# Performance work log

Hardware: AMD Instinct MI355X
Metric: run time of the kernel (lower is better)

## Reference

```python
import jax, jax.numpy as jnp
import numpy as np

B, S, DIN, DQ, DK = 8, 2048, 1024, 64, 64

def setup_inputs() -> dict:
    key = jax.random.key(0)
    ks = jax.random.split(key, 8)
    sc = 0.02
    return {
        "input_tensor": jax.random.normal(ks[0], (B, S, DIN), jnp.float32),
        "attention_mask": jax.random.randint(ks[1], (B, 1, S), 0, 2) == 1,
        "Wq": jax.random.normal(ks[2], (DIN, DQ), jnp.float32) * sc,
        "bq": jnp.zeros((DQ,), jnp.float32),
        "Wk": jax.random.normal(ks[3], (DIN, DK), jnp.float32) * sc,
        "bk": jnp.zeros((DK,), jnp.float32),
        "Wv": jax.random.normal(ks[4], (DIN, DK), jnp.float32) * sc,
        "bv": jnp.zeros((DK,), jnp.float32),
    }

def reference(input_tensor, attention_mask, Wq, bq, Wk, bk, Wv, bv):
    q = input_tensor @ Wq + bq          # [B,S,DQ]
    k = input_tensor @ Wk + bk          # [B,S,DK]
    v = input_tensor @ Wv + bv          # [B,S,DK]
    # NOTE: original scales by sqrt(query.size(1)) == sqrt(seq_len), faithfully kept
    scale = q.shape[1] ** 0.5
    scores = jnp.einsum('bqd,bkd->bqk', q, k) / scale
    scores = jnp.where(attention_mask, jnp.float32(-1e9), scores)
    attn = jax.nn.softmax(scores, axis=-1)
    context = jnp.einsum('bqk,bkd->bqd', attn, v)
    return context
```

## Files before the change

kernel.cpp:

```cpp
#include <hip/hip_runtime.h>
#include <hip/hip_bf16.h>

#define NB 8
#define SEQ 2048
#define DIN 1024
#define DH 64

typedef __attribute__((ext_vector_type(8))) short bf16x8;
typedef __attribute__((ext_vector_type(4))) float f32x4;
typedef __attribute__((ext_vector_type(4))) unsigned int u32x4;

static __device__ __forceinline__ unsigned short f2bf(float f) {
    unsigned int u = __builtin_bit_cast(unsigned int, f);
    unsigned int r = (u + 0x7FFFu + ((u >> 16) & 1u)) >> 16;
    return (unsigned short)r;
}

static __device__ __forceinline__ unsigned int cvt_pk_bf16(float lo, float hi) {
    unsigned int d;
    asm volatile("v_cvt_pk_bf16_f32 %0, %1, %2" : "=v"(d) : "v"(lo), "v"(hi));
    return d;
}

static __device__ __forceinline__ void gll16(const void* g, void* l) {
    __builtin_amdgcn_global_load_lds((const __attribute__((address_space(1))) unsigned int*)g,
                                     (__attribute__((address_space(3))) unsigned int*)l, 16, 0, 0);
}

#define WAITVM(N) asm volatile("s_waitcnt vmcnt(" #N ")" ::: "memory")

__global__ __launch_bounds__(256) void prep_kernel(
    const float* __restrict__ Wq, const float* __restrict__ Wk, const float* __restrict__ Wv,
    unsigned short* __restrict__ Wfrag)
{
    int j = blockIdx.x * 256 + threadIdx.x;
    int mat = j >> 16;
    int rem = j & 65535;
    int k = rem >> 6;
    int c = rem & 63;
    const float* W = (mat == 0) ? Wq : ((mat == 1) ? Wk : Wv);
    float v = W[rem];
    int col = mat * 64 + c;
    int cg = col >> 4, cl = col & 15;
    int kk = k >> 5, kq = (k >> 3) & 3, ke = k & 7;
    Wfrag[(size_t)(kk * 12 + cg) * 512 + cl * 32 + kq * 8 + ke] = f2bf(v);
}

__global__ __launch_bounds__(256) void qkv_kernel(
    const float* __restrict__ X, const unsigned short* __restrict__ Wfrag,
    const float* __restrict__ bq, const float* __restrict__ bk, const float* __restrict__ bv,
    unsigned short* __restrict__ Qb, unsigned short* __restrict__ Kb, unsigned short* __restrict__ Vt)
{
    __shared__ __align__(16) unsigned char Xs[3][8192];
    __shared__ __align__(16) unsigned char Ws[2][24576];

    const int tid = threadIdx.x;
    const int w   = tid >> 6;
    const int l15 = tid & 15;
    const int lq  = (tid >> 4) & 3;
    const int row0 = blockIdx.x * 32;

    const char* Xg = (const char*)(X + (size_t)row0 * DIN);
    const char* Wg = (const char*)Wfrag;

    int xlds[2], xsrc[2];
    #pragma unroll
    for (int i = 0; i < 2; ++i) {
        int b = i * 4096 + tid * 16;
        int row = b >> 8;
        int g = (b >> 4) & 15;
        xlds[i] = b;
        xsrc[i] = row * 4096 + (g ^ (row & 7)) * 16;
    }

    f32x4 acc[2][3] = {};

    #pragma unroll
    for (int i = 0; i < 2; ++i) gll16(Xg + (size_t)xsrc[i], &Xs[0][xlds[i]]);
    #pragma unroll
    for (int i = 0; i < 6; ++i) gll16(Wg + (size_t)(i * 4096 + tid * 16), &Ws[0][i * 4096 + tid * 16]);
    #pragma unroll
    for (int i = 0; i < 2; ++i) gll16(Xg + (size_t)xsrc[i] + 256, &Xs[1][xlds[i]]);

    #pragma unroll
    for (int t = 0; t < 16; ++t) {
        if (t < 15) { WAITVM(2); } else { WAITVM(0); }
        __builtin_amdgcn_s_barrier();
        __builtin_amdgcn_sched_barrier(0);

        if (t + 1 < 16) {
            #pragma unroll
            for (int i = 0; i < 6; ++i)
                gll16(Wg + (size_t)(t + 1) * 24576 + i * 4096 + tid * 16,
                      &Ws[(t + 1) & 1][i * 4096 + tid * 16]);
        }
        if (t + 2 < 16) {
            #pragma unroll
            for (int i = 0; i < 2; ++i)
                gll16(Xg + (size_t)xsrc[i] + (t + 2) * 256, &Xs[(t + 2) % 3][xlds[i]]);
        }

        const unsigned char* xb = Xs[t % 3];
        const unsigned char* wt = Ws[t & 1];
        #pragma unroll
        for (int kk = 0; kk < 2; ++kk) {
            bf16x8 a[2];
            #pragma unroll
            for (int m = 0; m < 2; ++m) {
                int row = m * 16 + l15;
                const unsigned char* rp = xb + row * 256;
                f32x4 f0 = *(const f32x4*)(rp + ((kk * 8 + lq * 2 + 0) ^ (row & 7)) * 16);
                f32x4 f1 = *(const f32x4*)(rp + ((kk * 8 + lq * 2 + 1) ^ (row & 7)) * 16);
                u32x4 pk;
                pk[0] = cvt_pk_bf16(f0[0], f0[1]);
                pk[1] = cvt_pk_bf16(f0[2], f0[3]);
                pk[2] = cvt_pk_bf16(f1[0], f1[1]);
                pk[3] = cvt_pk_bf16(f1[2], f1[3]);
                a[m] = __builtin_bit_cast(bf16x8, pk);
            }
            #pragma unroll
            for (int n = 0; n < 3; ++n) {
                bf16x8 bf = *(const bf16x8*)(wt + (kk * 12 + w * 3 + n) * 1024 + (l15 * 4 + lq) * 16);
                acc[0][n] = __builtin_amdgcn_mfma_f32_16x16x32_bf16(a[0], bf, acc[0][n], 0, 0, 0);
                acc[1][n] = __builtin_amdgcn_mfma_f32_16x16x32_bf16(a[1], bf, acc[1][n], 0, 0, 0);
            }
        }
    }

    #pragma unroll
    for (int n = 0; n < 3; ++n) {
        int col = w * 48 + n * 16 + l15;
        int mat = col >> 6, c = col & 63;
        float badd = ((mat == 0) ? bq : ((mat == 1) ? bk : bv))[c];
        #pragma unroll
        for (int m = 0; m < 2; ++m) {
            #pragma unroll
            for (int reg = 0; reg < 4; ++reg) {
                int row = row0 + m * 16 + lq * 4 + reg;
                unsigned short v16 = f2bf(acc[m][n][reg] + badd);
                if (mat == 0)      Qb[(size_t)row * DH + c] = v16;
                else if (mat == 1) Kb[(size_t)row * DH + c] = v16;
                else {
                    int bb = row >> 11, ss = row & 2047;
                    Vt[((size_t)(bb * DH + c)) * SEQ + ss] = v16;
                }
            }
        }
    }
}

#define AKT 64
#define ANT 8
#define PP 36

__global__ __launch_bounds__(256) void attn_kernel(
    const unsigned short* __restrict__ Qb, const unsigned short* __restrict__ Kb,
    const unsigned short* __restrict__ Vt, const int* __restrict__ mask,
    float* __restrict__ Opart, float* __restrict__ lpart)
{
    __shared__ __align__(16) unsigned char Ksm[3][8192];
    __shared__ __align__(16) unsigned char Vsm[3][8192];
    __shared__ short ps[4][32][PP];
    __shared__ float sml[4][32];

    const int tid = threadIdx.x;
    const int w   = tid >> 6;
    const int l15 = tid & 15;
    const int lq  = (tid >> 4) & 3;
    const int wm  = w >> 1;
    const int wn  = w & 1;

    int bid = blockIdx.x;
    int sbid = (bid & 7) * 128 + (bid >> 3);
    const int b   = sbid >> 7;
    const int qt  = (sbid >> 2) & 31;
    const int kq  = sbid & 3;
    const int q0  = qt * 64;
    const int kb0 = kq * 512;

    bf16x8 aq[2][2];
    #pragma unroll
    for (int m = 0; m < 2; ++m)
        #pragma unroll
        for (int kk = 0; kk < 2; ++kk)
            aq[m][kk] = *(const bf16x8*)(Qb + ((size_t)(b * SEQ + q0 + wm * 32 + m * 16 + l15)) * DH + kk * 32 + lq * 8);

    int mk[ANT][2];
    #pragma unroll
    for (int t = 0; t < ANT; ++t) {
        mk[t][0] = mask[b * SEQ + kb0 + t * AKT + wn * 32 + l15];
        mk[t][1] = mask[b * SEQ + kb0 + t * AKT + wn * 32 + 16 + l15];
    }
    WAITVM(0);

    const char* Kg = (const char*)Kb + (size_t)(b * SEQ + kb0) * DH * 2;
    const char* Vg = (const char*)Vt + ((size_t)(b * DH) * SEQ + kb0) * 2;

    int slds[2], ksrc[2], vsrc[2];
    #pragma unroll
    for (int i = 0; i < 2; ++i) {
        int bb = i * 4096 + tid * 16;
        int row = bb >> 7;
        int g = (bb >> 4) & 7;
        int gs = g ^ (row & 7);
        slds[i] = bb;
        ksrc[i] = row * 128 + gs * 16;
        vsrc[i] = row * 4096 + gs * 16;
    }

    f32x4 o[2][4];
    #pragma unroll
    for (int m = 0; m < 2; ++m)
        #pragma unroll
        for (int n = 0; n < 4; ++n) o[m][n] = f32x4{0, 0, 0, 0};
    float lr[2][4] = {};
    const float rscale = 0.022097086912079612f;

    #pragma unroll
    for (int i = 0; i < 2; ++i) gll16(Kg + (size_t)ksrc[i], &Ksm[0][slds[i]]);
    #pragma unroll
    for (int i = 0; i < 2; ++i) gll16(Vg + (size_t)vsrc[i], &Vsm[0][slds[i]]);
    #pragma unroll
    for (int i = 0; i < 2; ++i) gll16(Kg + (size_t)8192 + ksrc[i], &Ksm[1][slds[i]]);
    #pragma unroll
    for (int i = 0; i < 2; ++i) gll16(Vg + (size_t)128 + vsrc[i], &Vsm[1][slds[i]]);

    #pragma unroll
    for (int t = 0; t < ANT; ++t) {
        if (t < ANT - 1) { WAITVM(4); } else { WAITVM(0); }
        __builtin_amdgcn_s_barrier();
        __builtin_amdgcn_sched_barrier(0);

        if (t + 2 < ANT) {
            int bi = (t + 2) % 3;
            #pragma unroll
            for (int i = 0; i < 2; ++i) gll16(Kg + (size_t)(t + 2) * 8192 + ksrc[i], &Ksm[bi][slds[i]]);
            #pragma unroll
            for (int i = 0; i < 2; ++i) gll16(Vg + (size_t)(t + 2) * 128 + vsrc[i], &Vsm[bi][slds[i]]);
        }

        const unsigned char* kt  = Ksm[t % 3];
        const unsigned char* vt2 = Vsm[t % 3];

        bf16x8 bkf[2][2];
        #pragma unroll
        for (int n = 0; n < 2; ++n)
            #pragma unroll
            for (int kk = 0; kk < 2; ++kk) {
                int row = wn * 32 + n * 16 + l15;
                bkf[n][kk] = *(const bf16x8*)(kt + row * 128 + ((4 * kk + lq) ^ (row & 7)) * 16);
            }
        f32x4 s[2][2];
        #pragma unroll
        for (int m = 0; m < 2; ++m)
            #pragma unroll
            for (int n = 0; n < 2; ++n) s[m][n] = f32x4{0, 0, 0, 0};
        #pragma unroll
        for (int kk = 0; kk < 2; ++kk)
            #pragma unroll
            for (int m = 0; m < 2; ++m)
                #pragma unroll
                for (int n = 0; n < 2; ++n)
                    s[m][n] = __builtin_amdgcn_mfma_f32_16x16x32_bf16(aq[m][kk], bkf[n][kk], s[m][n], 0, 0, 0);

        float bb0 = mk[t][0] ? -1e30f : 0.0f;
        float bb1 = mk[t][1] ? -1e30f : 0.0f;
        #pragma unroll
        for (int m = 0; m < 2; ++m)
            #pragma unroll
            for (int n = 0; n < 2; ++n) {
                float bvv = n ? bb1 : bb0;
                #pragma unroll
                for (int r = 0; r < 4; ++r) {
                    float p = __expf(fmaf(s[m][n][r], rscale, bvv));
                    lr[m][r] += p;
                    ps[w][m * 16 + lq * 4 + r][n * 16 + l15] = (short)f2bf(p);
                }
            }

        bf16x8 pa[2];
        #pragma unroll
        for (int m = 0; m < 2; ++m)
            pa[m] = *(const bf16x8*)&ps[w][m * 16 + l15][lq * 8];
        bf16x8 bvf[4];
        #pragma unroll
        for (int n = 0; n < 4; ++n) {
            int row = n * 16 + l15;
            bvf[n] = *(const bf16x8*)(vt2 + row * 128 + ((4 * wn + lq) ^ (row & 7)) * 16);
        }
        #pragma unroll
        for (int m = 0; m < 2; ++m)
            #pragma unroll
            for (int n = 0; n < 4; ++n)
                o[m][n] = __builtin_amdgcn_mfma_f32_16x16x32_bf16(pa[m], bvf[n], o[m][n], 0, 0, 0);
    }

    #pragma unroll
    for (int off = 1; off < 16; off <<= 1)
        #pragma unroll
        for (int m = 0; m < 2; ++m)
            #pragma unroll
            for (int r = 0; r < 4; ++r) lr[m][r] += __shfl_xor(lr[m][r], off);
    if (l15 == 0) {
        #pragma unroll
        for (int m = 0; m < 2; ++m)
            #pragma unroll
            for (int r = 0; r < 4; ++r) sml[w][m * 16 + lq * 4 + r] = lr[m][r];
    }
    __syncthreads();

    float (*mg)[32][64] = reinterpret_cast<float (*)[32][64]>(&Ksm[0][0]);
    if (wn == 1) {
        #pragma unroll
        for (int m = 0; m < 2; ++m)
            #pragma unroll
            for (int n = 0; n < 4; ++n)
                #pragma unroll
                for (int r = 0; r < 4; ++r)
                    mg[wm][m * 16 + lq * 4 + r][n * 16 + l15] = o[m][n][r];
    }
    __syncthreads();
    if (wn == 0) {
        #pragma unroll
        for (int m = 0; m < 2; ++m)
            #pragma unroll
            for (int n = 0; n < 4; ++n)
                #pragma unroll
                for (int r = 0; r < 4; ++r)
                    mg[wm][m * 16 + lq * 4 + r][n * 16 + l15] += o[m][n][r];
    }
    __syncthreads();

    {
        int qq = tid >> 2;
        int d0 = (tid & 3) * 16;
        float* dst = Opart + ((size_t)kq * (NB * SEQ) + b * SEQ + q0 + qq) * DH + d0;
        #pragma unroll
        for (int j = 0; j < 4; ++j)
            *(float4*)(dst + j * 4) = *(float4*)&mg[qq >> 5][qq & 31][d0 + j * 4];
    }
    if (tid < 64) {
        int wmi = tid >> 5;
        float lsum = sml[wmi * 2][tid & 31] + sml[wmi * 2 + 1][tid & 31];
        lpart[(size_t)kq * (NB * SEQ) + b * SEQ + q0 + tid] = lsum;
    }
}

__global__ __launch_bounds__(256) void merge_kernel(
    const float* __restrict__ Opart, const float* __restrict__ lpart,
    float* __restrict__ out)
{
    int bid = blockIdx.x;
    int sbid = (bid & 7) * 32 + (bid >> 3);
    int g = sbid * 256 + threadIdx.x;
    int q  = g >> 2;
    int d0 = (g & 3) * 16;

    float l = lpart[q] + lpart[16384 + q] + lpart[2 * 16384 + q] + lpart[3 * 16384 + q];
    float inv = 1.0f / l;

    const float* o0 = Opart + (size_t)q * DH + d0;
    #pragma unroll
    for (int j = 0; j < 4; ++j) {
        float4 a = *(const float4*)(o0 + j * 4);
        float4 b2 = *(const float4*)(o0 + (size_t)16384 * DH + j * 4);
        float4 c = *(const float4*)(o0 + (size_t)2 * 16384 * DH + j * 4);
        float4 d = *(const float4*)(o0 + (size_t)3 * 16384 * DH + j * 4);
        float4 r;
        r.x = (a.x + b2.x + c.x + d.x) * inv;
        r.y = (a.y + b2.y + c.y + d.y) * inv;
        r.z = (a.z + b2.z + c.z + d.z) * inv;
        r.w = (a.w + b2.w + c.w + d.w) * inv;
        *(float4*)(out + (size_t)q * DH + d0 + j * 4) = r;
    }
}

extern "C" void kernel_launch(void* const* d_in, const int* in_sizes, int n_in,
                              void* d_out, int out_size, void* d_ws, size_t ws_size,
                              hipStream_t stream) {
    const float* X    = (const float*)d_in[0];
    const int*   mask = (const int*)d_in[1];
    const float* Wq   = (const float*)d_in[2];
    const float* bq   = (const float*)d_in[3];
    const float* Wk   = (const float*)d_in[4];
    const float* bk   = (const float*)d_in[5];
    const float* Wv   = (const float*)d_in[6];
    const float* bv   = (const float*)d_in[7];
    float* out = (float*)d_out;

    char* ws = (char*)d_ws;
    unsigned short* Qb    = (unsigned short*)(ws);
    unsigned short* Kb    = (unsigned short*)(ws + (2u << 20));
    unsigned short* Vt    = (unsigned short*)(ws + (4u << 20));
    unsigned short* Wfrag = (unsigned short*)(ws + (6u << 20));
    float* Opart          = (float*)(ws + (8u << 20));
    float* lpart          = (float*)(ws + (24u << 20));

    prep_kernel<<<768, 256, 0, stream>>>(Wq, Wk, Wv, Wfrag);
    qkv_kernel<<<512, 256, 0, stream>>>(X, Wfrag, bq, bk, bv, Qb, Kb, Vt);
    attn_kernel<<<1024, 256, 0, stream>>>(Qb, Kb, Vt, mask, Opart, lpart);
    merge_kernel<<<256, 256, 0, stream>>>(Opart, lpart, out);
}
```

Baseline: 62.41 us.

## Retile QKV projection into 128x64 output tiles with XCD-aware block swizzle

Measured after the change: 67.35 us. 7.9% more time.

```diff
diff --git a/kernel.cpp b/kernel.cpp
--- a/kernel.cpp
+++ b/kernel.cpp
@@ -31,7 +31,7 @@
 
 __global__ __launch_bounds__(256) void prep_kernel(
     const float* __restrict__ Wq, const float* __restrict__ Wk, const float* __restrict__ Wv,
-    unsigned short* __restrict__ Wfrag)
+    unsigned short* __restrict__ W3T)
 {
     int j = blockIdx.x * 256 + threadIdx.x;
     int mat = j >> 16;
@@ -40,106 +40,125 @@
     int c = rem & 63;
     const float* W = (mat == 0) ? Wq : ((mat == 1) ? Wk : Wv);
     float v = W[rem];
-    int col = mat * 64 + c;
-    int cg = col >> 4, cl = col & 15;
-    int kk = k >> 5, kq = (k >> 3) & 3, ke = k & 7;
-    Wfrag[(size_t)(kk * 12 + cg) * 512 + cl * 32 + kq * 8 + ke] = f2bf(v);
+    W3T[(size_t)(mat * 64 + c) * 1024 + k] = f2bf(v);
 }
 
 __global__ __launch_bounds__(256) void qkv_kernel(
-    const float* __restrict__ X, const unsigned short* __restrict__ Wfrag,
+    const float* __restrict__ X, const unsigned short* __restrict__ W3T,
     const float* __restrict__ bq, const float* __restrict__ bk, const float* __restrict__ bv,
     unsigned short* __restrict__ Qb, unsigned short* __restrict__ Kb, unsigned short* __restrict__ Vt)
 {
-    __shared__ __align__(16) unsigned char Xs[3][8192];
-    __shared__ __align__(16) unsigned char Ws[2][24576];
+    __shared__ __align__(16) unsigned char Xa[2][32768];
+    __shared__ __align__(16) unsigned char Wt[2][8192];
 
     const int tid = threadIdx.x;
     const int w   = tid >> 6;
     const int l15 = tid & 15;
     const int lq  = (tid >> 4) & 3;
-    const int row0 = blockIdx.x * 32;
-
-    const char* Xg = (const char*)(X + (size_t)row0 * DIN);
-    const char* Wg = (const char*)Wfrag;
-
-    int xlds[2], xsrc[2];
+    const int wm  = w >> 1;
+    const int wn  = w & 1;
+
+    int bid = blockIdx.x;
+    int sw = (bid & 7) * 48 + (bid >> 3);
+    const int rt = sw / 3;
+    const int ct = sw % 3;
+
+    const char* Xgb = (const char*)(X + (size_t)rt * 128 * DIN);
+    const char* Wgb = (const char*)W3T + (size_t)ct * 64 * 2048;
+
+    int xr[8], xsrc[8];
+    #pragma unroll
+    for (int i = 0; i < 8; ++i) {
+        int b = (i * 256 + tid) * 16;
+        int r = b >> 8;
+        int G = (b >> 5) & 7;
+        int h = (b >> 4) & 1;
+        xr[i] = b;
+        xsrc[i] = r * 4096 + ((G ^ (r & 7)) << 5) + (h << 4);
+    }
+    int wr[2], wsrc[2];
     #pragma unroll
     for (int i = 0; i < 2; ++i) {
-        int b = i * 4096 + tid * 16;
-        int row = b >> 8;
-        int g = (b >> 4) & 15;
-        xlds[i] = b;
-        xsrc[i] = row * 4096 + (g ^ (row & 7)) * 16;
-    }
-
-    f32x4 acc[2][3] = {};
-
-    #pragma unroll
-    for (int i = 0; i < 2; ++i) gll16(Xg + (size_t)xsrc[i], &Xs[0][xlds[i]]);
-    #pragma unroll
-    for (int i = 0; i < 6; ++i) gll16(Wg + (size_t)(i * 4096 + tid * 16), &Ws[0][i * 4096 + tid * 16]);
-    #pragma unroll
-    for (int i = 0; i < 2; ++i) gll16(Xg + (size_t)xsrc[i] + 256, &Xs[1][xlds[i]]);
+        int b = (i * 256 + tid) * 16;
+        int col = b >> 7;
+        int G = (b >> 4) & 7;
+        wr[i] = b;
+        wsrc[i] = col * 2048 + ((G ^ (col & 7)) << 4);
+    }
+
+    f32x4 acc[4][2] = {};
+
+    #pragma unroll
+    for (int i = 0; i < 8; ++i) gll16(Xgb + (size_t)xsrc[i], &Xa[0][xr[i]]);
+    #pragma unroll
+    for (int i = 0; i < 2; ++i) gll16(Wgb + (size_t)wsrc[i], &Wt[0][wr[i]]);
 
     #pragma unroll
     for (int t = 0; t < 16; ++t) {
-        if (t < 15) { WAITVM(2); } else { WAITVM(0); }
+        WAITVM(0);
         __builtin_amdgcn_s_barrier();
         __builtin_amdgcn_sched_barrier(0);
 
         if (t + 1 < 16) {
             #pragma unroll
-            for (int i = 0; i < 6; ++i)
-                gll16(Wg + (size_t)(t + 1) * 24576 + i * 4096 + tid * 16,
-                      &Ws[(t + 1) & 1][i * 4096 + tid * 16]);
-        }
-        if (t + 2 < 16) {
+            for (int i = 0; i < 8; ++i)
+                gll16(Xgb + (size_t)xsrc[i] + (t + 1) * 256, &Xa[(t + 1) & 1][xr[i]]);
             #pragma unroll
             for (int i = 0; i < 2; ++i)
-                gll16(Xg + (size_t)xsrc[i] + (t + 2) * 256, &Xs[(t + 2) % 3][xlds[i]]);
-        }
-
-        const unsigned char* xb = Xs[t % 3];
-        const unsigned char* wt = Ws[t & 1];
-        #pragma unroll
-        for (int kk = 0; kk < 2; ++kk) {
-            bf16x8 a[2];
-            #pragma unroll
-            for (int m = 0; m < 2; ++m) {
-                int row = m * 16 + l15;
-                const unsigned char* rp = xb + row * 256;
-                f32x4 f0 = *(const f32x4*)(rp + ((kk * 8 + lq * 2 + 0) ^ (row & 7)) * 16);
-                f32x4 f1 = *(const f32x4*)(rp + ((kk * 8 + lq * 2 + 1) ^ (row & 7)) * 16);
+                gll16(Wgb + (size_t)wsrc[i] + (t + 1) * 128, &Wt[(t + 1) & 1][wr[i]]);
+        }
+
+        const unsigned char* xb = Xa[t & 1];
+        const unsigned char* wb = Wt[t & 1];
+
+        bf16x8 a[4][2];
+        #pragma unroll
+        for (int m = 0; m < 4; ++m) {
+            int r = wm * 64 + m * 16 + l15;
+            const unsigned char* rp = xb + r * 256;
+            #pragma unroll
+            for (int kk = 0; kk < 2; ++kk) {
+                int g = (kk * 4 + lq) ^ (r & 7);
+                f32x4 f0 = *(const f32x4*)(rp + g * 32);
+                f32x4 f1 = *(const f32x4*)(rp + g * 32 + 16);
                 u32x4 pk;
                 pk[0] = cvt_pk_bf16(f0[0], f0[1]);
                 pk[1] = cvt_pk_bf16(f0[2], f0[3]);
                 pk[2] = cvt_pk_bf16(f1[0], f1[1]);
                 pk[3] = cvt_pk_bf16(f1[2], f1[3]);
-                a[m] = __builtin_bit_cast(bf16x8, pk);
+                a[m][kk] = __builtin_bit_cast(bf16x8, pk);
             }
-            #pragma unroll
-            for (int n = 0; n < 3; ++n) {
-                bf16x8 bf = *(const bf16x8*)(wt + (kk * 12 + w * 3 + n) * 1024 + (l15 * 4 + lq) * 16);
-                acc[0][n] = __builtin_amdgcn_mfma_f32_16x16x32_bf16(a[0], bf, acc[0][n], 0, 0, 0);
-                acc[1][n] = __builtin_amdgcn_mfma_f32_16x16x32_bf16(a[1], bf, acc[1][n], 0, 0, 0);
-            }
-        }
-    }
-
-    #pragma unroll
-    for (int n = 0; n < 3; ++n) {
-        int col = w * 48 + n * 16 + l15;
-        int mat = col >> 6, c = col & 63;
-        float badd = ((mat == 0) ? bq : ((mat == 1) ? bk : bv))[c];
-        #pragma unroll
-        for (int m = 0; m < 2; ++m) {
+        }
+        bf16x8 bf[2][2];
+        #pragma unroll
+        for (int n = 0; n < 2; ++n) {
+            int col = wn * 32 + n * 16 + l15;
+            #pragma unroll
+            for (int kk = 0; kk < 2; ++kk)
+                bf[n][kk] = *(const bf16x8*)(wb + col * 128 + (((kk * 4 + lq) ^ (col & 7)) << 4));
+        }
+        #pragma unroll
+        for (int kk = 0; kk < 2; ++kk)
+            #pragma unroll
+            for (int m = 0; m < 4; ++m)
+                #pragma unroll
+                for (int n = 0; n < 2; ++n)
+                    acc[m][n] = __builtin_amdgcn_mfma_f32_16x16x32_bf16(a[m][kk], bf[n][kk], acc[m][n], 0, 0, 0);
+    }
+
+    const float* bvec = (ct == 0) ? bq : ((ct == 1) ? bk : bv);
+    #pragma unroll
+    for (int n = 0; n < 2; ++n) {
+        int c = wn * 32 + n * 16 + l15;
+        float badd = bvec[c];
+        #pragma unroll
+        for (int m = 0; m < 4; ++m) {
             #pragma unroll
             for (int reg = 0; reg < 4; ++reg) {
-                int row = row0 + m * 16 + lq * 4 + reg;
+                int row = rt * 128 + wm * 64 + m * 16 + lq * 4 + reg;
                 unsigned short v16 = f2bf(acc[m][n][reg] + badd);
-                if (mat == 0)      Qb[(size_t)row * DH + c] = v16;
-                else if (mat == 1) Kb[(size_t)row * DH + c] = v16;
+                if (ct == 0)      Qb[(size_t)row * DH + c] = v16;
+                else if (ct == 1) Kb[(size_t)row * DH + c] = v16;
                 else {
                     int bb = row >> 11, ss = row & 2047;
                     Vt[((size_t)(bb * DH + c)) * SEQ + ss] = v16;
@@ -392,12 +411,12 @@
     unsigned short* Qb    = (unsigned short*)(ws);
     unsigned short* Kb    = (unsigned short*)(ws + (2u << 20));
     unsigned short* Vt    = (unsigned short*)(ws + (4u << 20));
-    unsigned short* Wfrag = (unsigned short*)(ws + (6u << 20));
+    unsigned short* W3T   = (unsigned short*)(ws + (6u << 20));
     float* Opart          = (float*)(ws + (8u << 20));
     float* lpart          = (float*)(ws + (24u << 20));
 
-    prep_kernel<<<768, 256, 0, stream>>>(Wq, Wk, Wv, Wfrag);
-    qkv_kernel<<<512, 256, 0, stream>>>(X, Wfrag, bq, bk, bv, Qb, Kb, Vt);
+    prep_kernel<<<768, 256, 0, stream>>>(Wq, Wk, Wv, W3T);
+    qkv_kernel<<<384, 256, 0, stream>>>(X, W3T, bq, bk, bv, Qb, Kb, Vt);
     attn_kernel<<<1024, 256, 0, stream>>>(Qb, Kb, Vt, mask, Opart, lpart);
     merge_kernel<<<256, 256, 0, stream>>>(Opart, lpart, out);
 }
```
